# Kernel optimization log

Hardware: AMD Instinct MI355X
Metric: run time of the kernel (lower is better)

The kernel has to match this reference:

```python
import jax, jax.numpy as jnp
import numpy as np
from jax import lax

B, N, NUM_CLS_P1, MASK_DIM, PH, PW = 2, 19248, 81, 32, 138, 138
MAX_OUT, MAX_CLS_OUT = 300, 100
IOU_THR, SCORE_THR, SIGMA = 0.5, 0.3, 0.5


def setup_inputs() -> dict:
    key = jax.random.key(0)
    k1, k2, k3, k4, k5 = jax.random.split(key, 5)
    pred_offset = jax.random.normal(k1, (B, N, 4), jnp.float32) * 0.05
    # scale logits so softmax produces a realistic spread of scores above 0.3
    pred_cls = jax.random.normal(k2, (B, N, NUM_CLS_P1), jnp.float32) * 3.0
    pred_mask_coef = jax.random.normal(k3, (B, N, MASK_DIM), jnp.float32)
    pr = jax.random.uniform(k4, (N, 4), jnp.float32)
    ctr, wh = pr[:, :2], 0.05 + 0.2 * pr[:, 2:]
    priors = jnp.concatenate([ctr - wh / 2, ctr + wh / 2], axis=-1)  # [N,4] y1x1y2x2-ish
    proto_out = jax.random.normal(k5, (B, PH, PW, MASK_DIM), jnp.float32)
    return dict(pred_offset=pred_offset, pred_cls=pred_cls,
                pred_mask_coef=pred_mask_coef, priors=priors, proto_out=proto_out)


def _corners(b):
    # TF NMS normalizes unordered corners with min/max
    y1 = jnp.minimum(b[..., 0], b[..., 2]); y2 = jnp.maximum(b[..., 0], b[..., 2])
    x1 = jnp.minimum(b[..., 1], b[..., 3]); x2 = jnp.maximum(b[..., 1], b[..., 3])
    return y1, x1, y2, x2


def soft_nms(boxes, scores):
    # boxes [N,4], scores [N] -> (idx [K], score [K], valid [K]); valid is a prefix mask
    y1, x1, y2, x2 = _corners(boxes)
    area = (y2 - y1) * (x2 - x1)

    def step(s, _):
        i = jnp.argmax(s)
        sc = s[i]
        valid = sc > SCORE_THR  # TF NMSv5 selects strictly above score_threshold
        iy1 = jnp.maximum(y1, y1[i]); ix1 = jnp.maximum(x1, x1[i])
        iy2 = jnp.minimum(y2, y2[i]); ix2 = jnp.minimum(x2, x2[i])
        inter = jnp.maximum(iy2 - iy1, 0.0) * jnp.maximum(ix2 - ix1, 0.0)
        union = area + area[i] - inter
        iou = jnp.where((area > 0.0) & (area[i] > 0.0),
                        inter / jnp.where(union > 0.0, union, 1.0), 0.0)
        # Gaussian soft suppression below hard IoU threshold, hard zero above (TF semantics)
        w = jnp.where(iou <= IOU_THR, jnp.exp((-0.5 / SIGMA) * iou * iou), 0.0)
        s_new = (s * w).at[i].set(-jnp.inf)
        s_next = jnp.where(valid, s_new, s)  # freeze once below threshold (selection stops)
        return s_next, (i, sc, valid)

    _, (idx, sc, valid) = lax.scan(step, scores, None, length=MAX_CLS_OUT)
    return idx, sc, valid


def detect_one(boxes, cls_scores, coefs, proto):
    # boxes [N,4], cls_scores [N,C], coefs [N,D], proto [H,W,D]
    C = cls_scores.shape[1]
    idx, sc, valid = jax.vmap(lambda s: soft_nms(boxes, s))(cls_scores.T)  # [C,K]
    vf = valid.astype(boxes.dtype)
    sel_boxes = boxes[idx] * vf[..., None]                          # [C,K,4]
    sel_coefs = coefs[idx] * vf[..., None]                          # [C,K,D]
    sel_scores = jnp.where(valid, sc, 0.0)                          # [C,K]
    sel_classes = jnp.where(valid, jnp.arange(1, C + 1, dtype=boxes.dtype)[:, None], 0.0)
    flat_scores = sel_scores.reshape(-1)
    order = jnp.argsort(-flat_scores)[:MAX_OUT]
    out_boxes = sel_boxes.reshape(-1, 4)[order]
    out_coefs = sel_coefs.reshape(-1, sel_coefs.shape[-1])[order]
    out_classes = sel_classes.reshape(-1)[order]
    out_scores = flat_scores[order]
    masks = jax.nn.sigmoid(jnp.einsum('hwd,kd->khw', proto, out_coefs))  # [K,H,W]
    return out_boxes, out_classes, out_scores, masks


def reference(pred_offset, pred_cls, pred_mask_coef, priors, proto_out):
    box_decode = pred_offset + priors[None]                          # [B,N,4]
    probs = jax.nn.softmax(pred_cls, axis=-1)[..., 1:]               # drop background [B,N,C]
    boxes_o, classes_o, scores_o, masks_o = jax.vmap(detect_one)(
        box_decode, probs, pred_mask_coef, proto_out)
    # original slices the (C*K)-sized buffer with [:max_output_size] -> always 300 when any prior passes
    any_pass = jnp.any(jnp.max(probs, axis=-1) > SCORE_THR, axis=-1)
    num_det = jnp.where(any_pass, MAX_OUT, 0).astype(jnp.int32)
    return boxes_o, classes_o, scores_o, masks_o, num_det
```

## Files before the change

kernel.cpp:

```cpp
#include <hip/hip_runtime.h>
#include <cstdint>
#include <cstddef>

#define B_ 2
#define N_ 19248
#define NCLSP1_ 81
#define NCLS_ 80
#define MAXK_ 100
#define MAXOUT_ 300
#define PH_ 138
#define PW_ 138
#define PHW_ (PH_*PW_)
#define MD_ 32
#define NBC_ (B_*NCLS_)
#define CAP_ 768
#define SCORE_THR_ 0.3f
#define IOU_THR_ 0.5f

#define OUT_BOXES 0
#define OUT_CLS   2400
#define OUT_SCR   3000
#define OUT_MASKS 3600
#define OUT_NDET  11430000

#define OFF_CURSORS 0
#define OFF_ANYFLAG 2560
#define POOLSZ      (NBC_*CAP_)
#define OFF_PS      2576
#define OFF_PY1     (OFF_PS  + POOLSZ)
#define OFF_PX1     (OFF_PY1 + POOLSZ)
#define OFF_PY2     (OFF_PX1 + POOLSZ)
#define OFF_PX2     (OFF_PY2 + POOLSZ)
#define OFF_PA      (OFF_PX2 + POOLSZ)
#define OFF_PIDX    (OFF_PA  + POOLSZ)
#define OFF_NSCORE  (OFF_PIDX + POOLSZ)
#define OFF_NANCH   (OFF_NSCORE + NBC_*MAXK_)
#define OFF_SELC    (OFF_NANCH + NBC_*MAXK_)

__device__ __forceinline__ float wave_max_f32(float x) {
    int v = __float_as_int(x);
    int t;
    #define DPPMAX(ctrl, rm, bm) \
        t = __builtin_amdgcn_update_dpp(v, v, ctrl, rm, bm, false); \
        v = __float_as_int(fmaxf(__int_as_float(v), __int_as_float(t)));
    DPPMAX(0x111, 0xF, 0xF)
    DPPMAX(0x112, 0xF, 0xF)
    DPPMAX(0x114, 0xF, 0xE)
    DPPMAX(0x118, 0xF, 0xC)
    DPPMAX(0x142, 0xA, 0xF)
    DPPMAX(0x143, 0xC, 0xF)
    #undef DPPMAX
    return __int_as_float(__builtin_amdgcn_readlane(v, 63));
}

__device__ __forceinline__ float wave_sum_f32(float x) {
    int v = __float_as_int(x);
    int t;
    #define DPPSUM(ctrl, rm, bm) \
        t = __builtin_amdgcn_update_dpp(v, v, ctrl, rm, bm, false); \
        v = __float_as_int(__int_as_float(v) + __int_as_float(t));
    DPPSUM(0x111, 0xF, 0xF)
    DPPSUM(0x112, 0xF, 0xF)
    DPPSUM(0x114, 0xF, 0xE)
    DPPSUM(0x118, 0xF, 0xC)
    DPPSUM(0x142, 0xA, 0xF)
    DPPSUM(0x143, 0xC, 0xF)
    #undef DPPSUM
    return __int_as_float(__builtin_amdgcn_readlane(v, 63));
}

__global__ __launch_bounds__(256) void k_fused(const float* __restrict__ cls,
        const float* __restrict__ off4, const float* __restrict__ priors,
        int* __restrict__ cursors, int* __restrict__ anyflag,
        float* __restrict__ ps, float* __restrict__ py1, float* __restrict__ px1,
        float* __restrict__ py2, float* __restrict__ px2, float* __restrict__ pa,
        int* __restrict__ pidx) {
    int wid = (blockIdx.x * 256 + threadIdx.x) >> 6;
    int lane = threadIdx.x & 63;
    if (wid >= B_ * N_) return;
    int b = wid / N_;
    int n = wid - b * N_;
    const float* x = cls + (size_t)wid * NCLSP1_;
    float v1 = x[lane];
    float v2 = (lane <= 16) ? x[lane + 64] : -INFINITY;
    float mx = wave_max_f32(fmaxf(v1, v2));
    float e1 = expf(v1 - mx);
    float e2 = (lane <= 16) ? expf(v2 - mx) : 0.f;
    float sum = wave_sum_f32(e1 + e2);
    float p1 = e1 / sum;
    float p2 = e2 / sum;
    bool q1 = (lane >= 1) && (p1 > SCORE_THR_);
    bool q2 = (lane <= 16) && (p2 > SCORE_THR_);
    if (q1 | q2) {
        anyflag[b] = 1;
        float4 o  = *(const float4*)(off4 + (size_t)wid * 4);
        float4 pr = *(const float4*)(priors + (size_t)n * 4);
        float d0 = o.x + pr.x, d1 = o.y + pr.y, d2 = o.z + pr.z, d3 = o.w + pr.w;
        float y1 = fminf(d0, d2), y2 = fmaxf(d0, d2);
        float x1 = fminf(d1, d3), x2 = fmaxf(d1, d3);
        float ar = (y2 - y1) * (x2 - x1);
        if (q1) {
            int bc = b * NCLS_ + (lane - 1);
            int pos = atomicAdd(&cursors[bc * 16], 1);
            if (pos < CAP_) {
                int o0 = bc * CAP_ + pos;
                ps[o0] = p1; py1[o0] = y1; px1[o0] = x1;
                py2[o0] = y2; px2[o0] = x2; pa[o0] = ar; pidx[o0] = n;
            }
        }
        if (q2) {
            int bc = b * NCLS_ + (lane + 63);
            int pos = atomicAdd(&cursors[bc * 16], 1);
            if (pos < CAP_) {
                int o0 = bc * CAP_ + pos;
                ps[o0] = p2; py1[o0] = y1; px1[o0] = x1;
                py2[o0] = y2; px2[o0] = x2; pa[o0] = ar; pidx[o0] = n;
            }
        }
    }
}

template<int J>
__device__ __forceinline__ void nms_reg(int bc, int M, int lane,
        const float* __restrict__ ps, const float* __restrict__ py1,
        const float* __restrict__ px1, const float* __restrict__ py2,
        const float* __restrict__ px2, const float* __restrict__ pa,
        const int* __restrict__ pidx,
        float* __restrict__ nscore, int* __restrict__ nanchor) {
    int base = bc * CAP_;
    float s[J], y1[J], x1[J], y2[J], x2[J], a[J];
    int pid[J];
    #pragma unroll
    for (int j = 0; j < J; j++) {
        int m = lane + 64 * j;
        bool in = (m < M);
        s[j]  = in ? ps[base + m]  : -INFINITY;
        y1[j] = in ? py1[base + m] : 0.f;
        x1[j] = in ? px1[base + m] : 0.f;
        y2[j] = in ? py2[base + m] : 0.f;
        x2[j] = in ? px2[base + m] : 0.f;
        a[j]  = in ? pa[base + m]  : 0.f;
        pid[j] = in ? pidx[base + m] : 0;
    }
    for (int k = 0; k < MAXK_; k++) {
        float lm = s[0];
        #pragma unroll
        for (int j = 1; j < J; j++) lm = fmaxf(lm, s[j]);
        float maxv = wave_max_f32(lm);
        if (!(maxv > SCORE_THR_)) break;
        unsigned long long bb[J];
        #pragma unroll
        for (int j = 0; j < J; j++) bb[j] = __ballot(s[j] == maxv);
        int bsel = 0;
        #pragma unroll
        for (int j = J - 1; j >= 0; j--) if (bb[j]) bsel = 64 * j + (__ffsll((long long)bb[j]) - 1);
        int jsel = bsel >> 6, lsel = bsel & 63;
        float ty1 = y1[0], tx1 = x1[0], ty2 = y2[0], tx2 = x2[0], ta = a[0]; int tpd = pid[0];
        #pragma unroll
        for (int j = 1; j < J; j++) {
            if (j == jsel) { ty1 = y1[j]; tx1 = x1[j]; ty2 = y2[j]; tx2 = x2[j]; ta = a[j]; tpd = pid[j]; }
        }
        float by1 = __int_as_float(__builtin_amdgcn_readlane(__float_as_int(ty1), lsel));
        float bx1 = __int_as_float(__builtin_amdgcn_readlane(__float_as_int(tx1), lsel));
        float by2 = __int_as_float(__builtin_amdgcn_readlane(__float_as_int(ty2), lsel));
        float bx2 = __int_as_float(__builtin_amdgcn_readlane(__float_as_int(tx2), lsel));
        float ba  = __int_as_float(__builtin_amdgcn_readlane(__float_as_int(ta),  lsel));
        int   bpd = __builtin_amdgcn_readlane(tpd, lsel);
        if (lane == 0) {
            nscore[bc * MAXK_ + k] = maxv;
            nanchor[bc * MAXK_ + k] = bpd;
        }
        #pragma unroll
        for (int j = 0; j < J; j++) {
            int m = lane + 64 * j;
            float iy1 = fmaxf(y1[j], by1), ix1 = fmaxf(x1[j], bx1);
            float iy2 = fminf(y2[j], by2), ix2 = fminf(x2[j], bx2);
            float inter = fmaxf(iy2 - iy1, 0.f) * fmaxf(ix2 - ix1, 0.f);
            float un = a[j] + ba - inter;
            float r  = (un > 0.f) ? __builtin_amdgcn_rcpf(un) : 1.f;
            float iou = (a[j] > 0.f && ba > 0.f) ? inter * r : 0.f;
            float w = (iou <= IOU_THR_) ? __expf(-iou * iou) : 0.f;
            s[j] = (m == bsel) ? -INFINITY : s[j] * w;
        }
    }
}

__device__ void nms_glb(int bc, int M, int lane,
        float* __restrict__ ps, float* __restrict__ py1, float* __restrict__ px1,
        float* __restrict__ py2, float* __restrict__ px2, float* __restrict__ pa,
        const int* __restrict__ pidx,
        float* __restrict__ nscore, int* __restrict__ nanchor) {
    int base = bc * CAP_;
    float* S = ps + base; float* Y1 = py1 + base; float* X1 = px1 + base;
    float* Y2 = py2 + base; float* X2 = px2 + base; float* A = pa + base;
    float bvv = -INFINITY; int bii = 0x7FFFFFFF;
    for (int m = lane; m < M; m += 64) { float v = S[m]; if (v > bvv) { bvv = v; bii = m; } }
    #pragma unroll
    for (int off = 32; off > 0; off >>= 1) {
        float ov = __shfl_xor(bvv, off);
        int   oi = __shfl_xor(bii, off);
        if (ov > bvv || (ov == bvv && oi < bii)) { bvv = ov; bii = oi; }
    }
    for (int k = 0; k < MAXK_; k++) {
        float val = bvv;
        if (!(val > SCORE_THR_)) break;
        int bsel = bii;
        if (lane == 0) {
            nscore[bc * MAXK_ + k] = val;
            nanchor[bc * MAXK_ + k] = pidx[base + bsel];
        }
        float by1 = Y1[bsel], bx1 = X1[bsel], by2 = Y2[bsel], bx2 = X2[bsel], ba = A[bsel];
        bvv = -INFINITY; bii = 0x7FFFFFFF;
        for (int m = lane; m < M; m += 64) {
            float s0 = S[m];
            float ns;
            if (s0 == -INFINITY) {
                ns = s0;
            } else {
                float iy1 = fmaxf(Y1[m], by1), ix1 = fmaxf(X1[m], bx1);
                float iy2 = fminf(Y2[m], by2), ix2 = fminf(X2[m], bx2);
                float inter = fmaxf(iy2 - iy1, 0.f) * fmaxf(ix2 - ix1, 0.f);
                float am = A[m];
                float un = am + ba - inter;
                float iou = (am > 0.f && ba > 0.f) ? inter / (un > 0.f ? un : 1.f) : 0.f;
                float w = (iou <= IOU_THR_) ? __expf(-iou * iou) : 0.f;
                ns = (m == bsel) ? -INFINITY : s0 * w;
                S[m] = ns;
            }
            if (ns > bvv) { bvv = ns; bii = m; }
        }
        #pragma unroll
        for (int off = 32; off > 0; off >>= 1) {
            float ov = __shfl_xor(bvv, off);
            int   oi = __shfl_xor(bii, off);
            if (ov > bvv || (ov == bvv && oi < bii)) { bvv = ov; bii = oi; }
        }
    }
}

__global__ __launch_bounds__(64) void k_nms(const int* __restrict__ cursors,
        float* __restrict__ ps, float* __restrict__ py1, float* __restrict__ px1,
        float* __restrict__ py2, float* __restrict__ px2, float* __restrict__ pa,
        const int* __restrict__ pidx,
        float* __restrict__ nscore, int* __restrict__ nanchor) {
    int bc = blockIdx.x;
    int lane = threadIdx.x & 63;
    int M = cursors[bc * 16];
    if (M > CAP_) M = CAP_;
    for (int k = lane; k < MAXK_; k += 64) { nscore[bc * MAXK_ + k] = 0.f; nanchor[bc * MAXK_ + k] = 0; }
    if (M == 0) return;
    if (M <= 128) { nms_reg<2>(bc, M, lane, ps, py1, px1, py2, px2, pa, pidx, nscore, nanchor); return; }
    if (M <= 256) { nms_reg<4>(bc, M, lane, ps, py1, px1, py2, px2, pa, pidx, nscore, nanchor); return; }
    nms_glb(bc, M, lane, ps, py1, px1, py2, px2, pa, pidx, nscore, nanchor);
}

__global__ __launch_bounds__(1024) void k_rank(const float* __restrict__ nscore,
        const int* __restrict__ nanchor, const int* __restrict__ anyflag,
        const float* __restrict__ off4, const float* __restrict__ priors,
        const float* __restrict__ coef, float* __restrict__ out, float* __restrict__ selc) {
    int b = blockIdx.y;
    int tid = threadIdx.x;
    __shared__ unsigned long long key[NCLS_ * MAXK_];
    for (int i = tid; i < NCLS_ * MAXK_; i += 1024) {
        float s = nscore[b * (NCLS_ * MAXK_) + i];
        key[i] = ((unsigned long long)__float_as_uint(s) << 32)
               | (unsigned)(0xFFFFFFFFu - (unsigned)i);
    }
    __syncthreads();
    if (blockIdx.x == 0 && tid == 0) out[OUT_NDET + b] = anyflag[b] ? (float)MAXOUT_ : 0.f;

    int i = blockIdx.x * 1000 + tid;
    if (tid >= 1000 || i >= NCLS_ * MAXK_) return;
    unsigned long long mykey = key[i];

    int rank = 0;
    #pragma unroll
    for (int cg = 0; cg < NCLS_; cg += 8) {
        int lo0=0,lo1=0,lo2=0,lo3=0,lo4=0,lo5=0,lo6=0,lo7=0;
        int hi0=MAXK_,hi1=MAXK_,hi2=MAXK_,hi3=MAXK_,hi4=MAXK_,hi5=MAXK_,hi6=MAXK_,hi7=MAXK_;
        #pragma unroll
        for (int it = 0; it < 7; it++) {
            #define BSTEP(u, lo, hi) { \
                int mid = (lo + hi) >> 1; \
                if (lo < hi) { \
                    unsigned long long v = key[(cg + u) * MAXK_ + mid]; \
                    if (v > mykey) lo = mid + 1; else hi = mid; \
                } }
            BSTEP(0, lo0, hi0) BSTEP(1, lo1, hi1) BSTEP(2, lo2, hi2) BSTEP(3, lo3, hi3)
            BSTEP(4, lo4, hi4) BSTEP(5, lo5, hi5) BSTEP(6, lo6, hi6) BSTEP(7, lo7, hi7)
            #undef BSTEP
        }
        rank += lo0+lo1+lo2+lo3+lo4+lo5+lo6+lo7;
    }
    if (rank >= MAXOUT_) return;

    float s = __uint_as_float((unsigned)(mykey >> 32));
    bool valid = (s > 0.f);
    int c = i / MAXK_;
    int anchor = valid ? nanchor[b * (NCLS_ * MAXK_) + i] : 0;
    out[OUT_SCR + b * MAXOUT_ + rank] = valid ? s : 0.f;
    out[OUT_CLS + b * MAXOUT_ + rank] = valid ? (float)(c + 1) : 0.f;
    size_t gb = (size_t)b * N_ + anchor;
    #pragma unroll
    for (int t = 0; t < 4; t++) {
        float v = valid ? (off4[gb * 4 + t] + priors[(size_t)anchor * 4 + t]) : 0.f;
        out[OUT_BOXES + ((size_t)b * MAXOUT_ + rank) * 4 + t] = v;
    }
    #pragma unroll
    for (int d = 0; d < MD_; d++) {
        selc[((size_t)b * MAXOUT_ + rank) * MD_ + d] = valid ? coef[gb * MD_ + d] : 0.f;
    }
}

#define KCHUNK 75
__global__ __launch_bounds__(256) void k_masks(const float* __restrict__ proto,
        const float* __restrict__ selc, float* __restrict__ om) {
    int b = blockIdx.z;
    int k0 = blockIdx.y * KCHUNK;
    int p = blockIdx.x * 256 + threadIdx.x;
    __shared__ float cf[KCHUNK * MD_];
    for (int i = threadIdx.x; i < KCHUNK * MD_; i += 256)
        cf[i] = selc[((size_t)b * MAXOUT_ + k0) * MD_ + i];
    __syncthreads();
    if (p >= PHW_) return;
    const float4* pp = (const float4*)(proto + ((size_t)b * PHW_ + p) * MD_);
    float4 pr[8];
    #pragma unroll
    for (int i = 0; i < 8; i++) pr[i] = pp[i];
    float* ob = om + ((size_t)b * MAXOUT_ + k0) * PHW_ + p;
    for (int kk = 0; kk < KCHUNK; kk++) {
        const float4* cv = (const float4*)(cf + kk * MD_);
        float acc = 0.f;
        #pragma unroll
        for (int i = 0; i < 8; i++) {
            float4 c = cv[i];
            acc += pr[i].x * c.x + pr[i].y * c.y + pr[i].z * c.z + pr[i].w * c.w;
        }
        ob[(size_t)kk * PHW_] = 1.f / (1.f + expf(-acc));
    }
}

extern "C" void kernel_launch(void* const* d_in, const int* in_sizes, int n_in,
                              void* d_out, int out_size, void* d_ws, size_t ws_size,
                              hipStream_t stream) {
    const float* pred_offset = (const float*)d_in[0];
    const float* pred_cls    = (const float*)d_in[1];
    const float* pred_coef   = (const float*)d_in[2];
    const float* priors      = (const float*)d_in[3];
    const float* proto       = (const float*)d_in[4];
    float* out = (float*)d_out;
    float* ws  = (float*)d_ws;
    int*   wsi = (int*)d_ws;

    int*   cursors = wsi + OFF_CURSORS;
    int*   anyflag = wsi + OFF_ANYFLAG;
    float* ps      = ws  + OFF_PS;
    float* py1     = ws  + OFF_PY1;
    float* px1     = ws  + OFF_PX1;
    float* py2     = ws  + OFF_PY2;
    float* px2     = ws  + OFF_PX2;
    float* pa      = ws  + OFF_PA;
    int*   pidx    = wsi + OFF_PIDX;
    float* nscore  = ws  + OFF_NSCORE;
    int*   nanchor = wsi + OFF_NANCH;
    float* selc    = ws  + OFF_SELC;

    hipMemsetAsync(d_ws, 0, (OFF_ANYFLAG + 2) * 4, stream);

    k_fused<<<(B_ * N_ * 64 + 255) / 256, 256, 0, stream>>>(pred_cls, pred_offset, priors,
            cursors, anyflag, ps, py1, px1, py2, px2, pa, pidx);
    k_nms<<<NBC_, 64, 0, stream>>>(cursors, ps, py1, px1, py2, px2, pa, pidx,
                                   nscore, nanchor);
    k_rank<<<dim3(8, B_), 1024, 0, stream>>>(nscore, nanchor, anyflag,
                                             pred_offset, priors, pred_coef, out, selc);
    k_masks<<<dim3((PHW_ + 255) / 256, MAXOUT_ / KCHUNK, B_), 256, 0, stream>>>(proto, selc, out + OUT_MASKS);
}
```

Baseline: 154.0 us.

## Use fast exp, ballot anyflag write, max-reduce selection in register NMS, add J=8 path

Switches expf to __expf in the softmax and the sigmoid mask output, and issues the anyflag store once per wave instead of from every passing lane. In the register NMS, the selected box is now found with wave max reductions over masked values instead of ballot, ffs and readlane, and the selected area is recomputed from the box corners. A new nms_reg<8> path keeps classes with up to 512 candidates in registers rather than falling back to the global-memory loop. Risks: ties on the maximum score suppress every tied entry and merge their boxes by max, the anchor index travels as a float, fast exp changes rounding slightly, and J=8 raises register pressure.

```diff
diff --git a/kernel.cpp b/kernel.cpp
--- a/kernel.cpp
+++ b/kernel.cpp
@@ -84,15 +84,18 @@
     float v1 = x[lane];
     float v2 = (lane <= 16) ? x[lane + 64] : -INFINITY;
     float mx = wave_max_f32(fmaxf(v1, v2));
-    float e1 = expf(v1 - mx);
-    float e2 = (lane <= 16) ? expf(v2 - mx) : 0.f;
+    float e1 = __expf(v1 - mx);
+    float e2 = (lane <= 16) ? __expf(v2 - mx) : 0.f;
     float sum = wave_sum_f32(e1 + e2);
     float p1 = e1 / sum;
     float p2 = e2 / sum;
     bool q1 = (lane >= 1) && (p1 > SCORE_THR_);
     bool q2 = (lane <= 16) && (p2 > SCORE_THR_);
+    unsigned long long bq = __ballot(q1 | q2);
+    if (bq) {
+        if (lane == (__ffsll((long long)bq) - 1)) anyflag[b] = 1;
+    }
     if (q1 | q2) {
-        anyflag[b] = 1;
         float4 o  = *(const float4*)(off4 + (size_t)wid * 4);
         float4 pr = *(const float4*)(priors + (size_t)n * 4);
         float d0 = o.x + pr.x, d1 = o.y + pr.y, d2 = o.z + pr.z, d3 = o.w + pr.w;
@@ -128,8 +131,7 @@
         const int* __restrict__ pidx,
         float* __restrict__ nscore, int* __restrict__ nanchor) {
     int base = bc * CAP_;
-    float s[J], y1[J], x1[J], y2[J], x2[J], a[J];
-    int pid[J];
+    float s[J], y1[J], x1[J], y2[J], x2[J], a[J], pidf[J];
     #pragma unroll
     for (int j = 0; j < J; j++) {
         int m = lane + 64 * j;
@@ -140,7 +142,7 @@
         y2[j] = in ? py2[base + m] : 0.f;
         x2[j] = in ? px2[base + m] : 0.f;
         a[j]  = in ? pa[base + m]  : 0.f;
-        pid[j] = in ? pidx[base + m] : 0;
+        pidf[j] = in ? (float)pidx[base + m] : -1.f;
     }
     for (int k = 0; k < MAXK_; k++) {
         float lm = s[0];
@@ -148,31 +150,34 @@
         for (int j = 1; j < J; j++) lm = fmaxf(lm, s[j]);
         float maxv = wave_max_f32(lm);
         if (!(maxv > SCORE_THR_)) break;
-        unsigned long long bb[J];
-        #pragma unroll
-        for (int j = 0; j < J; j++) bb[j] = __ballot(s[j] == maxv);
-        int bsel = 0;
-        #pragma unroll
-        for (int j = J - 1; j >= 0; j--) if (bb[j]) bsel = 64 * j + (__ffsll((long long)bb[j]) - 1);
-        int jsel = bsel >> 6, lsel = bsel & 63;
-        float ty1 = y1[0], tx1 = x1[0], ty2 = y2[0], tx2 = x2[0], ta = a[0]; int tpd = pid[0];
+        bool sel[J];
+        #pragma unroll
+        for (int j = 0; j < J; j++) sel[j] = (s[j] == maxv);
+        float fy1 = sel[0] ? y1[0] : -INFINITY;
+        float fx1 = sel[0] ? x1[0] : -INFINITY;
+        float fy2 = sel[0] ? y2[0] : -INFINITY;
+        float fx2 = sel[0] ? x2[0] : -INFINITY;
+        float fpd = sel[0] ? pidf[0] : -1.f;
         #pragma unroll
         for (int j = 1; j < J; j++) {
-            if (j == jsel) { ty1 = y1[j]; tx1 = x1[j]; ty2 = y2[j]; tx2 = x2[j]; ta = a[j]; tpd = pid[j]; }
-        }
-        float by1 = __int_as_float(__builtin_amdgcn_readlane(__float_as_int(ty1), lsel));
-        float bx1 = __int_as_float(__builtin_amdgcn_readlane(__float_as_int(tx1), lsel));
-        float by2 = __int_as_float(__builtin_amdgcn_readlane(__float_as_int(ty2), lsel));
-        float bx2 = __int_as_float(__builtin_amdgcn_readlane(__float_as_int(tx2), lsel));
-        float ba  = __int_as_float(__builtin_amdgcn_readlane(__float_as_int(ta),  lsel));
-        int   bpd = __builtin_amdgcn_readlane(tpd, lsel);
+            fy1 = fmaxf(fy1, sel[j] ? y1[j] : -INFINITY);
+            fx1 = fmaxf(fx1, sel[j] ? x1[j] : -INFINITY);
+            fy2 = fmaxf(fy2, sel[j] ? y2[j] : -INFINITY);
+            fx2 = fmaxf(fx2, sel[j] ? x2[j] : -INFINITY);
+            fpd = fmaxf(fpd, sel[j] ? pidf[j] : -1.f);
+        }
+        float by1 = wave_max_f32(fy1);
+        float bx1 = wave_max_f32(fx1);
+        float by2 = wave_max_f32(fy2);
+        float bx2 = wave_max_f32(fx2);
+        float bpd = wave_max_f32(fpd);
+        float ba  = (by2 - by1) * (bx2 - bx1);
         if (lane == 0) {
             nscore[bc * MAXK_ + k] = maxv;
-            nanchor[bc * MAXK_ + k] = bpd;
+            nanchor[bc * MAXK_ + k] = (int)bpd;
         }
         #pragma unroll
         for (int j = 0; j < J; j++) {
-            int m = lane + 64 * j;
             float iy1 = fmaxf(y1[j], by1), ix1 = fmaxf(x1[j], bx1);
             float iy2 = fminf(y2[j], by2), ix2 = fminf(x2[j], bx2);
             float inter = fmaxf(iy2 - iy1, 0.f) * fmaxf(ix2 - ix1, 0.f);
@@ -180,7 +185,7 @@
             float r  = (un > 0.f) ? __builtin_amdgcn_rcpf(un) : 1.f;
             float iou = (a[j] > 0.f && ba > 0.f) ? inter * r : 0.f;
             float w = (iou <= IOU_THR_) ? __expf(-iou * iou) : 0.f;
-            s[j] = (m == bsel) ? -INFINITY : s[j] * w;
+            s[j] = sel[j] ? -INFINITY : s[j] * w;
         }
     }
 }
@@ -251,6 +256,7 @@
     if (M == 0) return;
     if (M <= 128) { nms_reg<2>(bc, M, lane, ps, py1, px1, py2, px2, pa, pidx, nscore, nanchor); return; }
     if (M <= 256) { nms_reg<4>(bc, M, lane, ps, py1, px1, py2, px2, pa, pidx, nscore, nanchor); return; }
+    if (M <= 512) { nms_reg<8>(bc, M, lane, ps, py1, px1, py2, px2, pa, pidx, nscore, nanchor); return; }
     nms_glb(bc, M, lane, ps, py1, px1, py2, px2, pa, pidx, nscore, nanchor);
 }
 
@@ -336,7 +342,7 @@
             float4 c = cv[i];
             acc += pr[i].x * c.x + pr[i].y * c.y + pr[i].z * c.z + pr[i].w * c.w;
         }
-        ob[(size_t)kk * PHW_] = 1.f / (1.f + expf(-acc));
+        ob[(size_t)kk * PHW_] = 1.f / (1.f + __expf(-acc));
     }
 }
 
```

Result: slower. 182.4 us (+18.4%).

## Pair two classes per NMS wave, use fast exp, skip invalid rank entries

Applied to the files above, without the earlier changes.

Each NMS wave now processes two classes together so their serial argmax/suppress chains interleave for ILP, and it adds an 8-wide register path for up to 512 candidates. Softmax and sigmoid switch to the fast __expf intrinsic. anyflag is written once per wave via a ballot instead of by every qualifying lane. Rank threads holding zero-score entries exit early, and the outputs are zeroed with memsets instead. Half as many NMS blocks run, so parallelism drops and imbalanced pairs wait on the slower class. The extra memsets add launches, and __expf may change numerics slightly.

```diff
diff --git a/kernel.cpp b/kernel.cpp
--- a/kernel.cpp
+++ b/kernel.cpp
@@ -84,15 +84,18 @@
     float v1 = x[lane];
     float v2 = (lane <= 16) ? x[lane + 64] : -INFINITY;
     float mx = wave_max_f32(fmaxf(v1, v2));
-    float e1 = expf(v1 - mx);
-    float e2 = (lane <= 16) ? expf(v2 - mx) : 0.f;
+    float e1 = __expf(v1 - mx);
+    float e2 = (lane <= 16) ? __expf(v2 - mx) : 0.f;
     float sum = wave_sum_f32(e1 + e2);
     float p1 = e1 / sum;
     float p2 = e2 / sum;
     bool q1 = (lane >= 1) && (p1 > SCORE_THR_);
     bool q2 = (lane <= 16) && (p2 > SCORE_THR_);
+    unsigned long long bq = __ballot(q1 | q2);
+    if (bq) {
+        if (lane == (__ffsll((long long)bq) - 1)) anyflag[b] = 1;
+    }
     if (q1 | q2) {
-        anyflag[b] = 1;
         float4 o  = *(const float4*)(off4 + (size_t)wid * 4);
         float4 pr = *(const float4*)(priors + (size_t)n * 4);
         float d0 = o.x + pr.x, d1 = o.y + pr.y, d2 = o.z + pr.z, d3 = o.w + pr.w;
@@ -121,36 +124,40 @@
 }
 
 template<int J>
-__device__ __forceinline__ void nms_reg(int bc, int M, int lane,
-        const float* __restrict__ ps, const float* __restrict__ py1,
-        const float* __restrict__ px1, const float* __restrict__ py2,
-        const float* __restrict__ px2, const float* __restrict__ pa,
-        const int* __restrict__ pidx,
-        float* __restrict__ nscore, int* __restrict__ nanchor) {
-    int base = bc * CAP_;
+struct NmsCls {
     float s[J], y1[J], x1[J], y2[J], x2[J], a[J];
     int pid[J];
-    #pragma unroll
-    for (int j = 0; j < J; j++) {
-        int m = lane + 64 * j;
-        bool in = (m < M);
-        s[j]  = in ? ps[base + m]  : -INFINITY;
-        y1[j] = in ? py1[base + m] : 0.f;
-        x1[j] = in ? px1[base + m] : 0.f;
-        y2[j] = in ? py2[base + m] : 0.f;
-        x2[j] = in ? px2[base + m] : 0.f;
-        a[j]  = in ? pa[base + m]  : 0.f;
-        pid[j] = in ? pidx[base + m] : 0;
-    }
-    for (int k = 0; k < MAXK_; k++) {
+
+    __device__ __forceinline__ void load(int base, int M, int lane,
+            const float* __restrict__ ps, const float* __restrict__ py1,
+            const float* __restrict__ px1, const float* __restrict__ py2,
+            const float* __restrict__ px2, const float* __restrict__ pa,
+            const int* __restrict__ pidx) {
+        #pragma unroll
+        for (int j = 0; j < J; j++) {
+            int m = lane + 64 * j;
+            bool in = (m < M);
+            s[j]  = in ? ps[base + m]  : -INFINITY;
+            y1[j] = in ? py1[base + m] : 0.f;
+            x1[j] = in ? px1[base + m] : 0.f;
+            y2[j] = in ? py2[base + m] : 0.f;
+            x2[j] = in ? px2[base + m] : 0.f;
+            a[j]  = in ? pa[base + m]  : 0.f;
+            pid[j] = in ? pidx[base + m] : 0;
+        }
+    }
+
+    __device__ __forceinline__ float localmax() const {
         float lm = s[0];
         #pragma unroll
         for (int j = 1; j < J; j++) lm = fmaxf(lm, s[j]);
-        float maxv = wave_max_f32(lm);
-        if (!(maxv > SCORE_THR_)) break;
+        return lm;
+    }
+
+    __device__ __forceinline__ int step(float maxv, bool act, int lane) {
         unsigned long long bb[J];
         #pragma unroll
-        for (int j = 0; j < J; j++) bb[j] = __ballot(s[j] == maxv);
+        for (int j = 0; j < J; j++) bb[j] = __ballot(act && (s[j] == maxv));
         int bsel = 0;
         #pragma unroll
         for (int j = J - 1; j >= 0; j--) if (bb[j]) bsel = 64 * j + (__ffsll((long long)bb[j]) - 1);
@@ -166,10 +173,6 @@
         float bx2 = __int_as_float(__builtin_amdgcn_readlane(__float_as_int(tx2), lsel));
         float ba  = __int_as_float(__builtin_amdgcn_readlane(__float_as_int(ta),  lsel));
         int   bpd = __builtin_amdgcn_readlane(tpd, lsel);
-        if (lane == 0) {
-            nscore[bc * MAXK_ + k] = maxv;
-            nanchor[bc * MAXK_ + k] = bpd;
-        }
         #pragma unroll
         for (int j = 0; j < J; j++) {
             int m = lane + 64 * j;
@@ -180,7 +183,34 @@
             float r  = (un > 0.f) ? __builtin_amdgcn_rcpf(un) : 1.f;
             float iou = (a[j] > 0.f && ba > 0.f) ? inter * r : 0.f;
             float w = (iou <= IOU_THR_) ? __expf(-iou * iou) : 0.f;
-            s[j] = (m == bsel) ? -INFINITY : s[j] * w;
+            float wm = act ? w : 1.f;
+            s[j] = (act && m == bsel) ? -INFINITY : s[j] * wm;
+        }
+        return bpd;
+    }
+};
+
+template<int J>
+__device__ __forceinline__ void nms_pair(int bc0, int M0, int bc1, int M1, int lane,
+        const float* __restrict__ ps, const float* __restrict__ py1,
+        const float* __restrict__ px1, const float* __restrict__ py2,
+        const float* __restrict__ px2, const float* __restrict__ pa,
+        const int* __restrict__ pidx,
+        float* __restrict__ nscore, int* __restrict__ nanchor) {
+    NmsCls<J> c0, c1;
+    c0.load(bc0 * CAP_, M0, lane, ps, py1, px1, py2, px2, pa, pidx);
+    c1.load(bc1 * CAP_, M1, lane, ps, py1, px1, py2, px2, pa, pidx);
+    for (int k = 0; k < MAXK_; k++) {
+        float mv0 = wave_max_f32(c0.localmax());
+        float mv1 = wave_max_f32(c1.localmax());
+        bool a0 = (mv0 > SCORE_THR_);
+        bool a1 = (mv1 > SCORE_THR_);
+        if (!a0 && !a1) break;
+        int pd0 = c0.step(mv0, a0, lane);
+        int pd1 = c1.step(mv1, a1, lane);
+        if (lane == 0) {
+            if (a0) { nscore[bc0 * MAXK_ + k] = mv0; nanchor[bc0 * MAXK_ + k] = pd0; }
+            if (a1) { nscore[bc1 * MAXK_ + k] = mv1; nanchor[bc1 * MAXK_ + k] = pd1; }
         }
     }
 }
@@ -243,15 +273,25 @@
         float* __restrict__ py2, float* __restrict__ px2, float* __restrict__ pa,
         const int* __restrict__ pidx,
         float* __restrict__ nscore, int* __restrict__ nanchor) {
-    int bc = blockIdx.x;
+    int bc0 = blockIdx.x;
+    int bc1 = blockIdx.x + NBC_ / 2;
     int lane = threadIdx.x & 63;
-    int M = cursors[bc * 16];
-    if (M > CAP_) M = CAP_;
-    for (int k = lane; k < MAXK_; k += 64) { nscore[bc * MAXK_ + k] = 0.f; nanchor[bc * MAXK_ + k] = 0; }
-    if (M == 0) return;
-    if (M <= 128) { nms_reg<2>(bc, M, lane, ps, py1, px1, py2, px2, pa, pidx, nscore, nanchor); return; }
-    if (M <= 256) { nms_reg<4>(bc, M, lane, ps, py1, px1, py2, px2, pa, pidx, nscore, nanchor); return; }
-    nms_glb(bc, M, lane, ps, py1, px1, py2, px2, pa, pidx, nscore, nanchor);
+    int M0 = cursors[bc0 * 16]; if (M0 > CAP_) M0 = CAP_;
+    int M1 = cursors[bc1 * 16]; if (M1 > CAP_) M1 = CAP_;
+    for (int k = lane; k < MAXK_; k += 64) {
+        nscore[bc0 * MAXK_ + k] = 0.f; nanchor[bc0 * MAXK_ + k] = 0;
+        nscore[bc1 * MAXK_ + k] = 0.f; nanchor[bc1 * MAXK_ + k] = 0;
+    }
+    int Mmax = (M0 > M1) ? M0 : M1;
+    if (Mmax == 0) return;
+    if (Mmax <= 512) {
+        if (Mmax <= 128)      nms_pair<2>(bc0, M0, bc1, M1, lane, ps, py1, px1, py2, px2, pa, pidx, nscore, nanchor);
+        else if (Mmax <= 256) nms_pair<4>(bc0, M0, bc1, M1, lane, ps, py1, px1, py2, px2, pa, pidx, nscore, nanchor);
+        else                  nms_pair<8>(bc0, M0, bc1, M1, lane, ps, py1, px1, py2, px2, pa, pidx, nscore, nanchor);
+        return;
+    }
+    if (M0 > 0) nms_glb(bc0, M0, lane, ps, py1, px1, py2, px2, pa, pidx, nscore, nanchor);
+    if (M1 > 0) nms_glb(bc1, M1, lane, ps, py1, px1, py2, px2, pa, pidx, nscore, nanchor);
 }
 
 __global__ __launch_bounds__(1024) void k_rank(const float* __restrict__ nscore,
@@ -272,6 +312,7 @@
     int i = blockIdx.x * 1000 + tid;
     if (tid >= 1000 || i >= NCLS_ * MAXK_) return;
     unsigned long long mykey = key[i];
+    if ((unsigned)(mykey >> 32) == 0u) return;
 
     int rank = 0;
     #pragma unroll
@@ -295,20 +336,19 @@
     if (rank >= MAXOUT_) return;
 
     float s = __uint_as_float((unsigned)(mykey >> 32));
-    bool valid = (s > 0.f);
     int c = i / MAXK_;
-    int anchor = valid ? nanchor[b * (NCLS_ * MAXK_) + i] : 0;
-    out[OUT_SCR + b * MAXOUT_ + rank] = valid ? s : 0.f;
-    out[OUT_CLS + b * MAXOUT_ + rank] = valid ? (float)(c + 1) : 0.f;
+    int anchor = nanchor[b * (NCLS_ * MAXK_) + i];
+    out[OUT_SCR + b * MAXOUT_ + rank] = s;
+    out[OUT_CLS + b * MAXOUT_ + rank] = (float)(c + 1);
     size_t gb = (size_t)b * N_ + anchor;
     #pragma unroll
     for (int t = 0; t < 4; t++) {
-        float v = valid ? (off4[gb * 4 + t] + priors[(size_t)anchor * 4 + t]) : 0.f;
+        float v = off4[gb * 4 + t] + priors[(size_t)anchor * 4 + t];
         out[OUT_BOXES + ((size_t)b * MAXOUT_ + rank) * 4 + t] = v;
     }
     #pragma unroll
     for (int d = 0; d < MD_; d++) {
-        selc[((size_t)b * MAXOUT_ + rank) * MD_ + d] = valid ? coef[gb * MD_ + d] : 0.f;
+        selc[((size_t)b * MAXOUT_ + rank) * MD_ + d] = coef[gb * MD_ + d];
     }
 }
 
@@ -336,7 +376,7 @@
             float4 c = cv[i];
             acc += pr[i].x * c.x + pr[i].y * c.y + pr[i].z * c.z + pr[i].w * c.w;
         }
-        ob[(size_t)kk * PHW_] = 1.f / (1.f + expf(-acc));
+        ob[(size_t)kk * PHW_] = 1.f / (1.f + __expf(-acc));
     }
 }
 
@@ -366,11 +406,13 @@
     float* selc    = ws  + OFF_SELC;
 
     hipMemsetAsync(d_ws, 0, (OFF_ANYFLAG + 2) * 4, stream);
+    hipMemsetAsync(out, 0, 3600 * 4, stream);
+    hipMemsetAsync(selc, 0, (size_t)B_ * MAXOUT_ * MD_ * 4, stream);
 
     k_fused<<<(B_ * N_ * 64 + 255) / 256, 256, 0, stream>>>(pred_cls, pred_offset, priors,
             cursors, anyflag, ps, py1, px1, py2, px2, pa, pidx);
-    k_nms<<<NBC_, 64, 0, stream>>>(cursors, ps, py1, px1, py2, px2, pa, pidx,
-                                   nscore, nanchor);
+    k_nms<<<NBC_ / 2, 64, 0, stream>>>(cursors, ps, py1, px1, py2, px2, pa, pidx,
+                                       nscore, nanchor);
     k_rank<<<dim3(8, B_), 1024, 0, stream>>>(nscore, nanchor, anyflag,
                                              pred_offset, priors, pred_coef, out, selc);
     k_masks<<<dim3((PHW_ + 255) / 256, MAXOUT_ / KCHUNK, B_), 256, 0, stream>>>(proto, selc, out + OUT_MASKS);
```

After: 233.1 us. 51.3% more time.
